# Kernel tuning notes

Hardware: AMD Instinct MI355X
Metric: run time of the kernel (lower is better)

Reference implementation:

```python
import jax, jax.numpy as jnp
import numpy as np


def setup_inputs() -> dict:
    key = jax.random.key(0)
    k1, k2, k3 = jax.random.split(key, 3)
    B, C, H, W = 8, 256, 96, 96
    x = jax.random.normal(k1, (B, C, H, W), dtype=jnp.float32)
    # Conv1d(dim, 4*dim, kernel_size=1) == per-position linear [4C, C] + bias [4C]
    weight = jax.random.normal(k2, (4 * C, C), dtype=jnp.float32) * 0.02
    bias = jax.random.normal(k3, (4 * C,), dtype=jnp.float32) * 0.02
    return {"x": x, "weight": weight, "bias": bias}


def reference(x, weight, bias):
    # SS2D_Mamba.forward_scan with direction='horizontal'
    B, C, H, W = x.shape
    # [B,C,H,W] -> [B*H, W, C]: each of the B*H rows is an independent sequence
    xs = x.transpose(0, 2, 3, 1).reshape(B * H, W, C)
    # param_gen (1x1 Conv1d): [N, W, 4C]
    params = jax.nn.sigmoid(jnp.einsum('nwc,oc->nwo', xs, weight) + bias)
    A, Bg, Cg, Dg = jnp.split(params, 4, axis=-1)  # each [N, W, C]

    # sequential selective scan over W: h = a*h + b*x ; y = c*h + d*x
    def step(h, inp):
        a_t, b_t, c_t, d_t, x_t = inp
        h = a_t * h + b_t * x_t
        y_t = c_t * h + d_t * x_t
        return h, y_t

    h0 = jnp.zeros((B * H, C), dtype=x.dtype)
    seq = (A.swapaxes(0, 1), Bg.swapaxes(0, 1), Cg.swapaxes(0, 1),
           Dg.swapaxes(0, 1), xs.swapaxes(0, 1))  # time-major [W, N, C]
    _, ys = jax.lax.scan(step, h0, seq)  # ys: [W, N, C]

    y = ys.swapaxes(0, 1).reshape(B, H, W, C).transpose(0, 3, 1, 2)  # [B,C,H,W]
    return y
```

## Files before the change

kernel.cpp:

```cpp
#include <hip/hip_runtime.h>


#define C_DIM 256
#define H_DIM 96
#define W_DIM 96
#define QW    24
#define NQ    4

typedef float f4 __attribute__((ext_vector_type(4)));

__device__ __forceinline__ float sigf(float z) {
  return __builtin_amdgcn_rcpf(1.0f + __builtin_amdgcn_exp2f(z * -1.44269504088896340736f));
}

__global__ void pack_w(const float* __restrict__ w, const float* __restrict__ bias,
                       f4* __restrict__ wTI, f4* __restrict__ bias4)
{
  const int t = blockIdx.x * 256 + threadIdx.x;
  const int k = t >> 8;
  const int c = t & 255;
  f4 v;
  v[0] = w[(size_t)(c      ) * C_DIM + k];
  v[1] = w[(size_t)(c + 256) * C_DIM + k];
  v[2] = w[(size_t)(c + 512) * C_DIM + k];
  v[3] = w[(size_t)(c + 768) * C_DIM + k];
  wTI[t] = v;
  if (k == 0) {
    f4 bb;
    bb[0] = bias[c];
    bb[1] = bias[c + 256];
    bb[2] = bias[c + 512];
    bb[3] = bias[c + 768];
    bias4[c] = bb;
  }
}

__global__ __launch_bounds__(256, 3) void ss2d_main(
    const float* __restrict__ x, const f4* __restrict__ wTI,
    const f4* __restrict__ bias4, float* __restrict__ y)
{
  __shared__ f4 lds[2][6 * 256];

  const int tid = threadIdx.x;
  const int nb  = blockIdx.x;
  const int b   = nb / H_DIM;
  const int h   = nb - b * H_DIM;

  const size_t rowoff = ((size_t)(b * C_DIM + tid) * H_DIM + h) * W_DIM;
  const float* xrow = x + rowoff;
  float*       yrow = y + rowoff;

  const f4 bv = bias4[tid];
  float hstate = 0.0f;

  auto stage = [&](int s, int q) {
    const int wbase = tid & ~63;
#pragma unroll
    for (int i = 0; i < 6; ++i) {
      const float* g = xrow + q * QW + i * 4;
      auto* l = (__attribute__((address_space(3))) void*)(
          (char*)(&lds[s][0]) + (size_t)(i * 256 + wbase) * 16);
      __builtin_amdgcn_global_load_lds(
          (const __attribute__((address_space(1))) void*)g, l, 16, 0, 0);
    }
  };

  stage(0, 0);

  for (int q = 0; q < NQ; ++q) {
    const int cur = q & 1;
    __syncthreads();
    if (q < NQ - 1) stage(cur ^ 1, q + 1);

    f4 acc[QW];
#pragma unroll
    for (int w = 0; w < QW; ++w) acc[w] = bv;

    const f4* ldsc = &lds[cur][0];
    const f4* wp   = wTI + tid;
#pragma unroll 4
    for (int k = 0; k < C_DIM; ++k) {
      const f4 wv = wp[(size_t)k * C_DIM];
#pragma unroll
      for (int p = 0; p < 6; ++p) {
        const f4 xq = ldsc[p * 256 + k];
#pragma unroll
        for (int u = 0; u < 4; ++u) {
          acc[p * 4 + u] += xq[u] * wv;
        }
      }
    }

    f4 xt[6];
#pragma unroll
    for (int p = 0; p < 6; ++p) xt[p] = ldsc[p * 256 + tid];

    f4 yo[6];
#pragma unroll
    for (int w = 0; w < QW; ++w) {
      const f4 lg = acc[w];
      const float a  = sigf(lg[0]);
      const float bb = sigf(lg[1]);
      const float cc = sigf(lg[2]);
      const float dd = sigf(lg[3]);
      const float xv = xt[w >> 2][w & 3];
      hstate = a * hstate + bb * xv;
      yo[w >> 2][w & 3] = cc * hstate + dd * xv;
    }

    f4* yq = (f4*)(yrow + q * QW);
#pragma unroll
    for (int i = 0; i < 6; ++i) yq[i] = yo[i];
  }
}

extern "C" void kernel_launch(void* const* d_in, const int* in_sizes, int n_in,
                              void* d_out, int out_size, void* d_ws, size_t ws_size,
                              hipStream_t stream)
{
  const float* x    = (const float*)d_in[0];
  const float* w    = (const float*)d_in[1];
  const float* bias = (const float*)d_in[2];
  float* y = (float*)d_out;

  f4* wTI   = (f4*)d_ws;
  f4* bias4 = (f4*)((char*)d_ws + (size_t)C_DIM * C_DIM * sizeof(f4));

  hipLaunchKernelGGL(pack_w, dim3(256), dim3(256), 0, stream, w, bias, wTI, bias4);
  hipLaunchKernelGGL(ss2d_main, dim3(8 * H_DIM), dim3(256), 0, stream,
                     x, wTI, bias4, y);
}
```

Baseline: 648.6 us.

## Compute param projection with bf16 MFMA and LDS-transposed gate exchange

Replaces the per-thread FP32 FMA projection with bf16 MFMA 16x16x32 instructions. The weight is pre-packed into bf16 MFMA B-fragment layout, and x is converted to bf16 in a swizzled LDS tile. Sigmoid gates are redistributed through LDS in two halves so each thread can run its channel's sequential scan. The aim is to move the dominant GEMM onto matrix cores, at the cost of bf16 rounding of inputs and weights, extra LDS traffic and syncs, and lower occupancy.

```diff
diff --git a/kernel.cpp b/kernel.cpp
--- a/kernel.cpp
+++ b/kernel.cpp
@@ -1,116 +1,161 @@
 #include <hip/hip_runtime.h>
 
 
-#define C_DIM 256
 #define H_DIM 96
 #define W_DIM 96
+#define C_DIM 256
 #define QW    24
 #define NQ    4
 
-typedef float f4 __attribute__((ext_vector_type(4)));
+typedef float f4  __attribute__((ext_vector_type(4)));
+typedef short s4v __attribute__((ext_vector_type(4)));
+typedef short s8v __attribute__((ext_vector_type(8)));
+
+__device__ __forceinline__ unsigned short f2bf(float f) {
+  union { float f; unsigned u; } v; v.f = f;
+  unsigned r = v.u + 0x7FFFu + ((v.u >> 16) & 1u);
+  return (unsigned short)(r >> 16);
+}
 
 __device__ __forceinline__ float sigf(float z) {
   return __builtin_amdgcn_rcpf(1.0f + __builtin_amdgcn_exp2f(z * -1.44269504088896340736f));
 }
 
-__global__ void pack_w(const float* __restrict__ w, const float* __restrict__ bias,
-                       f4* __restrict__ wTI, f4* __restrict__ bias4)
+__global__ void pack_w(const float* __restrict__ w, s8v* __restrict__ wp)
 {
-  const int t = blockIdx.x * 256 + threadIdx.x;
-  const int k = t >> 8;
-  const int c = t & 255;
-  f4 v;
-  v[0] = w[(size_t)(c      ) * C_DIM + k];
-  v[1] = w[(size_t)(c + 256) * C_DIM + k];
-  v[2] = w[(size_t)(c + 512) * C_DIM + k];
-  v[3] = w[(size_t)(c + 768) * C_DIM + k];
-  wTI[t] = v;
-  if (k == 0) {
-    f4 bb;
-    bb[0] = bias[c];
-    bb[1] = bias[c + 256];
-    bb[2] = bias[c + 512];
-    bb[3] = bias[c + 768];
-    bias4[c] = bb;
+  const int idx  = blockIdx.x * 256 + threadIdx.x;
+  const int lane = idx & 63;
+  const int s    = (idx >> 6) & 7;
+  const int tile = idx >> 9;
+  const int n    = tile * 16 + (lane & 15);
+  const int kb   = s * 32 + ((lane >> 4) & 3) * 4;
+  const float* wr = w + (size_t)n * C_DIM;
+  s8v v;
+#pragma unroll
+  for (int j = 0; j < 8; ++j) {
+    const int k = kb + (j & 3) + ((j >> 2) << 4);
+    v[j] = (short)f2bf(wr[k]);
   }
+  wp[idx] = v;
 }
 
-__global__ __launch_bounds__(256, 3) void ss2d_main(
-    const float* __restrict__ x, const f4* __restrict__ wTI,
-    const f4* __restrict__ bias4, float* __restrict__ y)
+__global__ __launch_bounds__(256, 2) void ss2d_mfma(
+    const float* __restrict__ x, const s8v* __restrict__ wp,
+    const float* __restrict__ bias, float* __restrict__ y)
 {
-  __shared__ f4 lds[2][6 * 256];
+  __shared__ char Ald[32 * 512];
+  __shared__ f4   plds[12 * 256];
 
-  const int tid = threadIdx.x;
-  const int nb  = blockIdx.x;
-  const int b   = nb / H_DIM;
-  const int h   = nb - b * H_DIM;
+  const int tid  = threadIdx.x;
+  const int lane = tid & 63;
+  const int wv   = tid >> 6;
+  const int nb   = blockIdx.x;
+  const int b    = nb / H_DIM;
+  const int h    = nb - b * H_DIM;
 
   const size_t rowoff = ((size_t)(b * C_DIM + tid) * H_DIM + h) * W_DIM;
   const float* xrow = x + rowoff;
   float*       yrow = y + rowoff;
 
-  const f4 bv = bias4[tid];
+#pragma unroll
+  for (int m = 24; m < 32; ++m)
+    *(short*)(Ald + m * 512 + ((tid * 2) ^ ((m & 7) << 3))) = 0;
+
+  float bcol[16];
+#pragma unroll
+  for (int nt = 0; nt < 16; ++nt)
+    bcol[nt] = bias[wv * 256 + nt * 16 + (lane & 15)];
+
+  f4 xq[6], xq2[6];
+#pragma unroll
+  for (int i = 0; i < 6; ++i) xq[i] = *(const f4*)(xrow + i * 4);
+
   float hstate = 0.0f;
-
-  auto stage = [&](int s, int q) {
-    const int wbase = tid & ~63;
-#pragma unroll
-    for (int i = 0; i < 6; ++i) {
-      const float* g = xrow + q * QW + i * 4;
-      auto* l = (__attribute__((address_space(3))) void*)(
-          (char*)(&lds[s][0]) + (size_t)(i * 256 + wbase) * 16);
-      __builtin_amdgcn_global_load_lds(
-          (const __attribute__((address_space(1))) void*)g, l, 16, 0, 0);
-    }
-  };
-
-  stage(0, 0);
+  const int m0   = lane & 15;
+  const int g    = lane >> 4;
+  const int rb0  = m0 * 512;
+  const int xorm = (m0 & 7) << 3;
 
   for (int q = 0; q < NQ; ++q) {
-    const int cur = q & 1;
+#pragma unroll
+    for (int m = 0; m < QW; ++m)
+      *(short*)(Ald + m * 512 + ((tid * 2) ^ ((m & 7) << 3))) =
+          (short)f2bf(xq[m >> 2][m & 3]);
+    if (q < NQ - 1) {
+#pragma unroll
+      for (int i = 0; i < 6; ++i)
+        xq2[i] = *(const f4*)(xrow + (q + 1) * QW + i * 4);
+    }
     __syncthreads();
-    if (q < NQ - 1) stage(cur ^ 1, q + 1);
 
-    f4 acc[QW];
+    f4 acc0[16], acc1[16];
 #pragma unroll
-    for (int w = 0; w < QW; ++w) acc[w] = bv;
-
-    const f4* ldsc = &lds[cur][0];
-    const f4* wp   = wTI + tid;
-#pragma unroll 4
-    for (int k = 0; k < C_DIM; ++k) {
-      const f4 wv = wp[(size_t)k * C_DIM];
+    for (int nt = 0; nt < 16; ++nt) {
+      const f4 iv = { bcol[nt], bcol[nt], bcol[nt], bcol[nt] };
+      acc0[nt] = iv; acc1[nt] = iv;
+    }
+    for (int s = 0; s < 8; ++s) {
+      const int kb = s * 64 + (g << 3);
+      const int x0 = kb ^ xorm;
+      const int x1 = (kb + 32) ^ xorm;
+      const s4v a0l = *(const s4v*)(Ald + rb0 + x0);
+      const s4v a0h = *(const s4v*)(Ald + rb0 + x1);
+      const s4v a1l = *(const s4v*)(Ald + 8192 + rb0 + x0);
+      const s4v a1h = *(const s4v*)(Ald + 8192 + rb0 + x1);
+      const s8v a0 = __builtin_shufflevector(a0l, a0h, 0,1,2,3,4,5,6,7);
+      const s8v a1 = __builtin_shufflevector(a1l, a1h, 0,1,2,3,4,5,6,7);
+      const s8v* wrow = wp + ((size_t)(wv * 16) * 8 + s) * 64 + lane;
 #pragma unroll
-      for (int p = 0; p < 6; ++p) {
-        const f4 xq = ldsc[p * 256 + k];
-#pragma unroll
-        for (int u = 0; u < 4; ++u) {
-          acc[p * 4 + u] += xq[u] * wv;
-        }
+      for (int nt = 0; nt < 16; ++nt) {
+        const s8v bf = wrow[(size_t)nt * 8 * 64];
+        acc0[nt] = __builtin_amdgcn_mfma_f32_16x16x32_bf16(a0, bf, acc0[nt], 0, 0, 0);
+        acc1[nt] = __builtin_amdgcn_mfma_f32_16x16x32_bf16(a1, bf, acc1[nt], 0, 0, 0);
       }
     }
 
-    f4 xt[6];
 #pragma unroll
-    for (int p = 0; p < 6; ++p) xt[p] = ldsc[p * 256 + tid];
+    for (int nt = 0; nt < 16; ++nt)
+#pragma unroll
+      for (int j = 0; j < 4; ++j) {
+        acc0[nt][j] = sigf(acc0[nt][j]);
+        acc1[nt][j] = sigf(acc1[nt][j]);
+      }
 
-    f4 yo[6];
 #pragma unroll
-    for (int w = 0; w < QW; ++w) {
-      const f4 lg = acc[w];
-      const float a  = sigf(lg[0]);
-      const float bb = sigf(lg[1]);
-      const float cc = sigf(lg[2]);
-      const float dd = sigf(lg[3]);
-      const float xv = xt[w >> 2][w & 3];
-      hstate = a * hstate + bb * xv;
-      yo[w >> 2][w & 3] = cc * hstate + dd * xv;
+    for (int half = 0; half < 2; ++half) {
+      __syncthreads();
+#pragma unroll
+      for (int nt = 0; nt < 16; ++nt) {
+        const int c = nt * 16 + m0;
+        float* base = (float*)&plds[0] + (size_t)c * 4 + wv;
+#pragma unroll
+        for (int j = 0; j < 4; ++j) {
+          const int w0 = 4 * g + j;
+          if (half == 0) {
+            if (w0 < 12) base[(size_t)w0 * 1024] = acc0[nt][j];
+          } else {
+            if (w0 >= 12) base[(size_t)(w0 - 12) * 1024] = acc0[nt][j];
+            const int w1 = 16 + 4 * g + j;
+            if (w1 < 24) base[(size_t)(w1 - 12) * 1024] = acc1[nt][j];
+          }
+        }
+      }
+      __syncthreads();
+      f4 yo[3];
+#pragma unroll
+      for (int wq = 0; wq < 12; ++wq) {
+        const f4 p = plds[wq * 256 + tid];
+        const int wg = half * 12 + wq;
+        const float xv = xq[wg >> 2][wg & 3];
+        hstate = p[0] * hstate + p[1] * xv;
+        yo[wq >> 2][wq & 3] = p[2] * hstate + p[3] * xv;
+      }
+#pragma unroll
+      for (int i = 0; i < 3; ++i)
+        *(f4*)(yrow + q * QW + half * 12 + i * 4) = yo[i];
     }
-
-    f4* yq = (f4*)(yrow + q * QW);
 #pragma unroll
-    for (int i = 0; i < 6; ++i) yq[i] = yo[i];
+    for (int i = 0; i < 6; ++i) xq[i] = xq2[i];
   }
 }
 
@@ -123,10 +168,9 @@
   const float* bias = (const float*)d_in[2];
   float* y = (float*)d_out;
 
-  f4* wTI   = (f4*)d_ws;
-  f4* bias4 = (f4*)((char*)d_ws + (size_t)C_DIM * C_DIM * sizeof(f4));
+  s8v* wp = (s8v*)d_ws;
 
-  hipLaunchKernelGGL(pack_w, dim3(256), dim3(256), 0, stream, w, bias, wTI, bias4);
-  hipLaunchKernelGGL(ss2d_main, dim3(8 * H_DIM), dim3(256), 0, stream,
-                     x, wTI, bias4, y);
+  hipLaunchKernelGGL(pack_w, dim3(128), dim3(256), 0, stream, w, wp);
+  hipLaunchKernelGGL(ss2d_mfma, dim3(8 * H_DIM), dim3(256), 0, stream,
+                     x, wp, bias, y);
 }
```

After: 887.2 us. +36.8%, slower.
